# Performance work log

Measured on AMD Instinct MI355X. Metric: run time of the kernel, lower is better.

The kernel has to match this reference:

```python
import jax, jax.numpy as jnp
import numpy as np

N_NODES = 100000
N_EDGES = 6400000
DIM_FEAT = 5


def setup_inputs() -> dict:
    key = jax.random.key(0)
    k1, k2, k3 = jax.random.split(key, 3)
    features = jax.random.normal(k1, (N_NODES, DIM_FEAT), dtype=jnp.float32)
    src = jax.random.randint(k2, (N_EDGES,), 0, N_NODES, dtype=jnp.int64)
    dst = jax.random.randint(k3, (N_EDGES,), 0, N_NODES, dtype=jnp.int64)
    return {"features": features, "src": src, "dst": dst}


def reference(features, src, dst):
    # copy_u('h','m') then sum('m','h'):
    # h_out[v] = sum over edges (u->v) of features[u]
    msgs = features[src]  # [E, F] gather
    h = jax.ops.segment_sum(msgs, dst, num_segments=N_NODES)  # [N, F]
    return h
```

## Files before the change

### kernel.cpp

```cpp
#include <hip/hip_runtime.h>
#include <hip/hip_bf16.h>


#define NN     100000
#define FD     5
#define NOUTT  (NN * FD)
#define NPS    32
#define NPS_SH 5
#define NB     3125
#define NSB    512
#define BLK    256

__device__ inline unsigned bf16rtn(float x) {
    unsigned u = __float_as_uint(x);
    u += 0x7fffu + ((u >> 16) & 1u);
    return u >> 16;
}
__device__ inline float lo16(unsigned v) { return __uint_as_float(v << 16); }
__device__ inline float hi16(unsigned v) { return __uint_as_float(v & 0xffff0000u); }

__global__ __launch_bounds__(BLK) void k2_hist(const int* __restrict__ dst,
                                               unsigned short* __restrict__ bh,
                                               int chunk) {
    __shared__ int h[NB];
    for (int b = threadIdx.x; b < NB; b += BLK) h[b] = 0;
    __syncthreads();
    long long e0 = (long long)blockIdx.x * chunk;
    const int4* d4 = (const int4*)(dst + e0);
    int n4 = chunk >> 2;
    for (int i = threadIdx.x; i < n4; i += BLK) {
        int4 d = d4[i];
        atomicAdd(&h[d.x >> NPS_SH], 1);
        atomicAdd(&h[d.y >> NPS_SH], 1);
        atomicAdd(&h[d.z >> NPS_SH], 1);
        atomicAdd(&h[d.w >> NPS_SH], 1);
    }
    __syncthreads();
    unsigned short* row = bh + (size_t)blockIdx.x * NB;
    for (int b = threadIdx.x; b < NB; b += BLK) row[b] = (unsigned short)h[b];
}

__global__ __launch_bounds__(BLK) void k3_scanblk(unsigned short* __restrict__ bh,
                                                  int* __restrict__ btot) {
    __shared__ int s[BLK];
    int b = blockIdx.x, t = threadIdx.x;
    int v0 = bh[(size_t)(2 * t)     * NB + b];
    int v1 = bh[(size_t)(2 * t + 1) * NB + b];
    int pair = v0 + v1;
    s[t] = pair;
    __syncthreads();
    for (int off = 1; off < BLK; off <<= 1) {
        int v = (t >= off) ? s[t - off] : 0;
        __syncthreads();
        s[t] += v;
        __syncthreads();
    }
    int base = s[t] - pair;
    bh[(size_t)(2 * t)     * NB + b] = (unsigned short)base;
    bh[(size_t)(2 * t + 1) * NB + b] = (unsigned short)(base + v0);
    if (t == BLK - 1) btot[b] = s[t];
}

#define VPT 13
__global__ __launch_bounds__(BLK) void k4_scanbkt(const int* __restrict__ btot,
                                                  int* __restrict__ bbase) {
    __shared__ int s[BLK];
    int t = threadIdx.x;
    int v[VPT], sum = 0;
#pragma unroll
    for (int k = 0; k < VPT; ++k) {
        int i = VPT * t + k;
        v[k] = (i < NB) ? btot[i] : 0;
        sum += v[k];
    }
    s[t] = sum;
    __syncthreads();
    for (int off = 1; off < BLK; off <<= 1) {
        int u = (t >= off) ? s[t - off] : 0;
        __syncthreads();
        s[t] += u;
        __syncthreads();
    }
    int run = s[t] - sum;
#pragma unroll
    for (int k = 0; k < VPT; ++k) {
        int i = VPT * t + k;
        if (i < NB) bbase[i] = run;
        run += v[k];
    }
}

__global__ __launch_bounds__(BLK) void k5_scatter(const int* __restrict__ src,
                                                  const int* __restrict__ dst,
                                                  const unsigned short* __restrict__ bh,
                                                  const int* __restrict__ bbase,
                                                  int* __restrict__ bdata, int chunk) {
    __shared__ int cur[NB];
    int blk = blockIdx.x;
    const unsigned short* row = bh + (size_t)blk * NB;
    for (int b = threadIdx.x; b < NB; b += BLK)
        cur[b] = bbase[b] + (int)row[b];
    __syncthreads();
    long long e0 = (long long)blk * chunk;
    const int4* d4 = (const int4*)(dst + e0);
    const int4* s4 = (const int4*)(src + e0);
    int n4 = chunk >> 2;
    for (int i = threadIdx.x; i < n4; i += BLK) {
        int4 d = d4[i];
        int4 s = s4[i];
        int vv[4] = {d.x, d.y, d.z, d.w};
        int uu[4] = {s.x, s.y, s.z, s.w};
#pragma unroll
        for (int j = 0; j < 4; ++j) {
            int b = vv[j] >> NPS_SH;
            int off = atomicAdd(&cur[b], 1);
            bdata[off] = (uu[j] << NPS_SH) | (vv[j] & (NPS - 1));
        }
    }
}

__global__ __launch_bounds__(BLK) void k1_pad(const float* __restrict__ f,
                                              uint4* __restrict__ fp) {
    int i = blockIdx.x * BLK + threadIdx.x;
    if (i < NN) {
        const float* r = f + (long long)i * FD;
        unsigned w0 = bf16rtn(r[0]), w1 = bf16rtn(r[1]), w2 = bf16rtn(r[2]);
        unsigned w3 = bf16rtn(r[3]), w4 = bf16rtn(r[4]);
        uint4 o;
        o.x = w0 | (w1 << 16);
        o.y = w2 | (w3 << 16);
        o.z = w4;
        o.w = 0u;
        fp[i] = o;
    }
}

#define UNR 8
__global__ __launch_bounds__(BLK) void k6_gather(const int* __restrict__ bdata,
                                                 const uint4* __restrict__ fp,
                                                 const int* __restrict__ bbase,
                                                 const int* __restrict__ btot,
                                                 float* __restrict__ out) {
    __shared__ float acc[NPS * FD];
    int t = threadIdx.x;
    if (t < NPS * FD) acc[t] = 0.f;
    __syncthreads();
    int bid = blockIdx.x;
    int b = bid >> 1, r = bid & 1;
    int base = bbase[b];
    int n = btot[b];
    int n0 = n >> 1;
    int s0 = base + (r ? n0 : 0);
    int cnt = r ? (n - n0) : n0;

    int i = t;
    for (; i + (UNR - 1) * BLK < cnt; i += UNR * BLK) {
        int   l[UNR];
        uint4 g[UNR];
#pragma unroll
        for (int k = 0; k < UNR; ++k) {
            int w = bdata[s0 + i + k * BLK];
            l[k] = w & (NPS - 1);
            g[k] = fp[w >> NPS_SH];
        }
        __builtin_amdgcn_sched_barrier(0);
#pragma unroll
        for (int k = 0; k < UNR; ++k) {
            float* p = acc + l[k] * FD;
            atomicAdd(&p[0], lo16(g[k].x));
            atomicAdd(&p[1], hi16(g[k].x));
            atomicAdd(&p[2], lo16(g[k].y));
            atomicAdd(&p[3], hi16(g[k].y));
            atomicAdd(&p[4], lo16(g[k].z));
        }
    }
    for (; i < cnt; i += BLK) {
        int w = bdata[s0 + i];
        int l = w & (NPS - 1);
        uint4 g = fp[w >> NPS_SH];
        float* p = acc + l * FD;
        atomicAdd(&p[0], lo16(g.x)); atomicAdd(&p[1], hi16(g.x));
        atomicAdd(&p[2], lo16(g.y)); atomicAdd(&p[3], hi16(g.y));
        atomicAdd(&p[4], lo16(g.z));
    }
    __syncthreads();
    if (t < NPS * FD)
        atomicAdd(&out[(size_t)b * NPS * FD + t], acc[t]);
}

__global__ void scatter_add_fallback(const float* __restrict__ features,
                                     const int* __restrict__ src,
                                     const int* __restrict__ dst,
                                     float* __restrict__ out, int n_edges) {
    int idx = blockIdx.x * blockDim.x + threadIdx.x;
    int stride = gridDim.x * blockDim.x;
    for (int e = idx; e < n_edges; e += stride) {
        int u = src[e], v = dst[e];
        const float* f = features + (long long)u * FD;
        float* o = out + (long long)v * FD;
#pragma unroll
        for (int k = 0; k < FD; ++k) atomicAdd(&o[k], f[k]);
    }
}

extern "C" void kernel_launch(void* const* d_in, const int* in_sizes, int n_in,
                              void* d_out, int out_size, void* d_ws, size_t ws_size,
                              hipStream_t stream) {
    const float* features = (const float*)d_in[0];
    const int*   src      = (const int*)d_in[1];
    const int*   dst      = (const int*)d_in[2];
    float* out = (float*)d_out;
    int n_edges = in_sizes[1];

    size_t o_bd = 0;
    size_t o_bh = o_bd + (size_t)n_edges * 4;
    size_t o_fp = o_bh;
    size_t sz_overlap = (size_t)NSB * NB * 2;
    size_t sz_fp = (size_t)NN * sizeof(uint4);
    if (sz_fp > sz_overlap) sz_overlap = sz_fp;
    size_t o_bb = o_bh + ((sz_overlap + 15) & ~(size_t)15);
    size_t o_bt = o_bb + (size_t)NB * 4;
    size_t need = o_bt + (size_t)NB * 4;

    bool fast = (out_size == NOUTT) && (in_sizes[0] == NOUTT) &&
                (n_edges % (NSB * 4) == 0) && (need <= ws_size);

    if (fast) {
        char* w = (char*)d_ws;
        int*            bdata = (int*)(w + o_bd);
        unsigned short* bhist = (unsigned short*)(w + o_bh);
        uint4*          fpad  = (uint4*)(w + o_fp);
        int*            bbase = (int*)(w + o_bb);
        int*            btot  = (int*)(w + o_bt);
        int chunk = n_edges / NSB;
        hipMemsetAsync(d_out, 0, (size_t)out_size * sizeof(float), stream);
        k2_hist  <<<NSB, BLK, 0, stream>>>(dst, bhist, chunk);
        k3_scanblk<<<NB, BLK, 0, stream>>>(bhist, btot);
        k4_scanbkt<<<1,  BLK, 0, stream>>>(btot, bbase);
        k5_scatter<<<NSB, BLK, 0, stream>>>(src, dst, bhist, bbase, bdata, chunk);
        k1_pad   <<<(NN + BLK - 1) / BLK, BLK, 0, stream>>>(features, fpad);
        k6_gather <<<2 * NB, BLK, 0, stream>>>(bdata, fpad, bbase, btot, out);
    } else {
        hipMemsetAsync(d_out, 0, (size_t)out_size * sizeof(float), stream);
        int grid = (n_edges + BLK - 1) / BLK;
        if (grid > 65535) grid = 65535;
        scatter_add_fallback<<<grid, BLK, 0, stream>>>(features, src, dst, out, n_edges);
    }
}
```

Before: 395.6 us.

## Use nontemporal vector loads, unroll hist/scatter, one gather block per bucket

The histogram and scatter kernels now issue four independent nontemporal 16-byte loads per thread before their shared-memory atomics, and the scatter writes its packed edge words with nontemporal stores. The gather kernel goes from two blocks per bucket to one, so each block writes its output slice directly and the output memset plus the global atomics disappear. The aim is more memory-level parallelism in the streaming passes and fewer launches and atomics at the end. In exchange the gather grid halves (3125 blocks), so each bucket's edges are handled by a single block and load balance may suffer.

```diff
diff --git a/kernel.cpp b/kernel.cpp
--- a/kernel.cpp
+++ b/kernel.cpp
@@ -11,6 +11,8 @@
 #define NSB    512
 #define BLK    256
 
+typedef int vint4 __attribute__((ext_vector_type(4)));
+
 __device__ inline unsigned bf16rtn(float x) {
     unsigned u = __float_as_uint(x);
     u += 0x7fffu + ((u >> 16) & 1u);
@@ -26,14 +28,28 @@
     for (int b = threadIdx.x; b < NB; b += BLK) h[b] = 0;
     __syncthreads();
     long long e0 = (long long)blockIdx.x * chunk;
-    const int4* d4 = (const int4*)(dst + e0);
+    const vint4* d4 = (const vint4*)(dst + e0);
     int n4 = chunk >> 2;
-    for (int i = threadIdx.x; i < n4; i += BLK) {
-        int4 d = d4[i];
-        atomicAdd(&h[d.x >> NPS_SH], 1);
-        atomicAdd(&h[d.y >> NPS_SH], 1);
-        atomicAdd(&h[d.z >> NPS_SH], 1);
-        atomicAdd(&h[d.w >> NPS_SH], 1);
+    int i = threadIdx.x;
+    for (; i + 3 * BLK < n4; i += 4 * BLK) {
+        vint4 d0 = __builtin_nontemporal_load(&d4[i]);
+        vint4 d1 = __builtin_nontemporal_load(&d4[i + BLK]);
+        vint4 d2 = __builtin_nontemporal_load(&d4[i + 2 * BLK]);
+        vint4 d3 = __builtin_nontemporal_load(&d4[i + 3 * BLK]);
+        __builtin_amdgcn_sched_barrier(0);
+        atomicAdd(&h[d0[0] >> NPS_SH], 1); atomicAdd(&h[d0[1] >> NPS_SH], 1);
+        atomicAdd(&h[d0[2] >> NPS_SH], 1); atomicAdd(&h[d0[3] >> NPS_SH], 1);
+        atomicAdd(&h[d1[0] >> NPS_SH], 1); atomicAdd(&h[d1[1] >> NPS_SH], 1);
+        atomicAdd(&h[d1[2] >> NPS_SH], 1); atomicAdd(&h[d1[3] >> NPS_SH], 1);
+        atomicAdd(&h[d2[0] >> NPS_SH], 1); atomicAdd(&h[d2[1] >> NPS_SH], 1);
+        atomicAdd(&h[d2[2] >> NPS_SH], 1); atomicAdd(&h[d2[3] >> NPS_SH], 1);
+        atomicAdd(&h[d3[0] >> NPS_SH], 1); atomicAdd(&h[d3[1] >> NPS_SH], 1);
+        atomicAdd(&h[d3[2] >> NPS_SH], 1); atomicAdd(&h[d3[3] >> NPS_SH], 1);
+    }
+    for (; i < n4; i += BLK) {
+        vint4 d = __builtin_nontemporal_load(&d4[i]);
+        atomicAdd(&h[d[0] >> NPS_SH], 1); atomicAdd(&h[d[1] >> NPS_SH], 1);
+        atomicAdd(&h[d[2] >> NPS_SH], 1); atomicAdd(&h[d[3] >> NPS_SH], 1);
     }
     __syncthreads();
     unsigned short* row = bh + (size_t)blockIdx.x * NB;
@@ -102,19 +118,42 @@
         cur[b] = bbase[b] + (int)row[b];
     __syncthreads();
     long long e0 = (long long)blk * chunk;
-    const int4* d4 = (const int4*)(dst + e0);
-    const int4* s4 = (const int4*)(src + e0);
+    const vint4* d4 = (const vint4*)(dst + e0);
+    const vint4* s4 = (const vint4*)(src + e0);
     int n4 = chunk >> 2;
-    for (int i = threadIdx.x; i < n4; i += BLK) {
-        int4 d = d4[i];
-        int4 s = s4[i];
-        int vv[4] = {d.x, d.y, d.z, d.w};
-        int uu[4] = {s.x, s.y, s.z, s.w};
+    int i = threadIdx.x;
+    for (; i + 3 * BLK < n4; i += 4 * BLK) {
+        vint4 d[4], s[4];
+#pragma unroll
+        for (int k = 0; k < 4; ++k) {
+            d[k] = __builtin_nontemporal_load(&d4[i + k * BLK]);
+            s[k] = __builtin_nontemporal_load(&s4[i + k * BLK]);
+        }
+        __builtin_amdgcn_sched_barrier(0);
+#pragma unroll
+        for (int k = 0; k < 4; ++k) {
+#pragma unroll
+            for (int j = 0; j < 4; ++j) {
+                int vv = d[k][j];
+                int uu = s[k][j];
+                int b = vv >> NPS_SH;
+                int off = atomicAdd(&cur[b], 1);
+                __builtin_nontemporal_store((uu << NPS_SH) | (vv & (NPS - 1)),
+                                            &bdata[off]);
+            }
+        }
+    }
+    for (; i < n4; i += BLK) {
+        vint4 d = __builtin_nontemporal_load(&d4[i]);
+        vint4 s = __builtin_nontemporal_load(&s4[i]);
 #pragma unroll
         for (int j = 0; j < 4; ++j) {
-            int b = vv[j] >> NPS_SH;
+            int vv = d[j];
+            int uu = s[j];
+            int b = vv >> NPS_SH;
             int off = atomicAdd(&cur[b], 1);
-            bdata[off] = (uu[j] << NPS_SH) | (vv[j] & (NPS - 1));
+            __builtin_nontemporal_store((uu << NPS_SH) | (vv & (NPS - 1)),
+                                        &bdata[off]);
         }
     }
 }
@@ -145,21 +184,17 @@
     int t = threadIdx.x;
     if (t < NPS * FD) acc[t] = 0.f;
     __syncthreads();
-    int bid = blockIdx.x;
-    int b = bid >> 1, r = bid & 1;
+    int b = blockIdx.x;
     int base = bbase[b];
     int n = btot[b];
-    int n0 = n >> 1;
-    int s0 = base + (r ? n0 : 0);
-    int cnt = r ? (n - n0) : n0;
 
     int i = t;
-    for (; i + (UNR - 1) * BLK < cnt; i += UNR * BLK) {
+    for (; i + (UNR - 1) * BLK < n; i += UNR * BLK) {
         int   l[UNR];
         uint4 g[UNR];
 #pragma unroll
         for (int k = 0; k < UNR; ++k) {
-            int w = bdata[s0 + i + k * BLK];
+            int w = __builtin_nontemporal_load(&bdata[base + i + k * BLK]);
             l[k] = w & (NPS - 1);
             g[k] = fp[w >> NPS_SH];
         }
@@ -174,8 +209,8 @@
             atomicAdd(&p[4], lo16(g[k].z));
         }
     }
-    for (; i < cnt; i += BLK) {
-        int w = bdata[s0 + i];
+    for (; i < n; i += BLK) {
+        int w = __builtin_nontemporal_load(&bdata[base + i]);
         int l = w & (NPS - 1);
         uint4 g = fp[w >> NPS_SH];
         float* p = acc + l * FD;
@@ -184,8 +219,7 @@
         atomicAdd(&p[4], lo16(g.z));
     }
     __syncthreads();
-    if (t < NPS * FD)
-        atomicAdd(&out[(size_t)b * NPS * FD + t], acc[t]);
+    if (t < NPS * FD) out[(size_t)b * NPS * FD + t] = acc[t];
 }
 
 __global__ void scatter_add_fallback(const float* __restrict__ features,
@@ -233,15 +267,14 @@
         int*            bbase = (int*)(w + o_bb);
         int*            btot  = (int*)(w + o_bt);
         int chunk = n_edges / NSB;
-        hipMemsetAsync(d_out, 0, (size_t)out_size * sizeof(float), stream);
         k2_hist  <<<NSB, BLK, 0, stream>>>(dst, bhist, chunk);
         k3_scanblk<<<NB, BLK, 0, stream>>>(bhist, btot);
         k4_scanbkt<<<1,  BLK, 0, stream>>>(btot, bbase);
         k5_scatter<<<NSB, BLK, 0, stream>>>(src, dst, bhist, bbase, bdata, chunk);
         k1_pad   <<<(NN + BLK - 1) / BLK, BLK, 0, stream>>>(features, fpad);
-        k6_gather <<<2 * NB, BLK, 0, stream>>>(bdata, fpad, bbase, btot, out);
+        k6_gather <<<NB, BLK, 0, stream>>>(bdata, fpad, bbase, btot, out);
     } else {
-        hipMemsetAsync(d_out, 0, (size_t)out_size * sizeof(float), stream);
+        (void)hipMemsetAsync(d_out, 0, (size_t)out_size * sizeof(float), stream);
         int grid = (n_edges + BLK - 1) / BLK;
         if (grid > 65535) grid = 65535;
         scatter_add_fallback<<<grid, BLK, 0, stream>>>(features, src, dst, out, n_edges);
```

After: 528.6 us. 33.6% more time.
